# Kernel optimization log

Hardware: AMD Instinct MI355X
Metric: run time of the kernel (lower is better)

The kernel has to match this reference:

```python
import jax, jax.numpy as jnp
import numpy as np

BIT_W = 8   # config.bit_wt
BIT_A = 8   # config.bit_act (activations sliced 2 bits at a time)
STRIDE = (1, 1)
PAD = 1


def _conv(a, w):
    # NCHW input, OIHW weight, stride 1, symmetric padding 1 (matches wrapped Conv2d)
    return jax.lax.conv_general_dilated(
        a, w, window_strides=STRIDE, padding=[(PAD, PAD), (PAD, PAD)],
        dimension_numbers=("NCHW", "OIHW", "NCHW"))


def setup_inputs() -> dict:
    key = jax.random.key(0)
    k1, k2, k3 = jax.random.split(key, 3)
    x = jax.random.normal(k1, (64, 64, 56, 56), dtype=jnp.float32)
    weight = jax.random.normal(k2, (64, 64, 3, 3), dtype=jnp.float32)
    bias = jax.random.normal(k3, (64,), dtype=jnp.float32)
    scale_a = jnp.full((1,), 20.0, dtype=jnp.float32)      # conv_q.scale
    scale_w = jnp.full((1,), 20.0, dtype=jnp.float32)      # wrapped_module.weight_scale
    zero_point = jnp.full((1,), -128.0, dtype=jnp.float32)  # conv_q.zero_point
    return {"x": x, "weight": weight, "bias": bias,
            "scale_a": scale_a, "scale_w": scale_w, "zero_point": zero_point}


def reference(x, weight, bias, scale_a, scale_w, zero_point):
    sa = scale_a[0]
    sw = scale_w[0]
    zp = zero_point[0]
    # activation quantization: round(x*scale_a - zero_point), clamp to [0, 2^bit_act - 1]
    q_in = jnp.clip(jnp.round(x * sa - zp), 0.0, 2.0 ** BIT_A - 1.0)
    # weight quantization: round(w * scale_w), interpreted in two's complement
    q_w = jnp.round(weight * sw)
    w_off = q_w + 2.0 ** BIT_W  # (w + (1 << bit_weight)) before bit masking

    acc = jnp.zeros((), dtype=jnp.float32)
    for ba in range(BIT_A // 2):
        # 2-bit activation slice: (a >> 2*ba) & 3
        a_sl = jnp.mod(jnp.floor(q_in / (4.0 ** ba)), 4.0)
        for bw in range(BIT_W):
            # weight bit bw: ((w + 2^B) >> bw) & 1
            w_bit = jnp.mod(jnp.floor(w_off / (2.0 ** bw)), 2.0)
            r = _conv(a_sl, w_bit)
            sgn = -1.0 if bw == BIT_W - 1 else 1.0  # MSB = sign bit (two's complement)
            acc = acc + sgn * (2.0 ** (2 * ba + bw)) * r

    # zero-point correction: conv(ones * zp, q_w) added back (no-op when zp == 0)
    acc = acc + zp * _conv(jnp.ones_like(q_in), q_w)

    out = acc / (sw * sa) + bias[None, :, None, None]
    return out
```

## Files before the change

kernel.cpp:

```cpp
#include <hip/hip_runtime.h>


typedef int v4i __attribute__((ext_vector_type(4)));

#define QA_ROW   3712
#define QA_IMG   215296
#define QA_BYTES 13778944

__global__ __launch_bounds__(64) void prep_wq(const float* __restrict__ wt,
                                              const float* __restrict__ sw_p,
                                              signed char* __restrict__ w8,
                                              int* __restrict__ Qtc,
                                              int* __restrict__ Qraw) {
  const int o = blockIdx.x;
  const int i = threadIdx.x;
  const float sw = sw_p[0];
  const float* wp = wt + (size_t)(o * 64 + i) * 9;
  int q[9];
#pragma unroll
  for (int k = 0; k < 9; ++k) q[k] = (int)rintf(wp[k] * sw);
#pragma unroll
  for (int k = 0; k < 9; ++k)
    w8[(o * 9 + k) * 64 + i] = (signed char)(q[k] & 255);
#pragma unroll
  for (int k = 0; k < 9; ++k) {
    int stc = (int)(signed char)(q[k] & 255);
    int srw = q[k];
#pragma unroll
    for (int off = 32; off; off >>= 1) {
      stc += __shfl_xor(stc, off);
      srw += __shfl_xor(srw, off);
    }
    if (i == 0) { Qtc[o * 9 + k] = stc; Qraw[o * 9 + k] = srw; }
  }
}

__global__ __launch_bounds__(256) void quant_a(const float* __restrict__ x,
                                               const float* __restrict__ sa_p,
                                               const float* __restrict__ zp_p,
                                               signed char* __restrict__ qa) {
  __shared__ int ldsbuf[1904];
  signed char* lds = (signed char*)ldsbuf;
  const int bx = blockIdx.x;
  const int n = blockIdx.y;
  const int t = threadIdx.x;
  const float sa = sa_p[0], zp = zp_p[0];
  const float* xim = x + (size_t)n * 200704;
  const int h0 = bx * 2;

#pragma unroll
  for (int it = 0; it < 7; ++it) {
    const int idx = t + 256 * it;
    const int r = idx >= 896;
    const int rem = idx - 896 * r;
    const int c = (rem * 2341) >> 15;
    const int w4 = rem - c * 14;
    const float4 v = *(const float4*)(xim + (size_t)c * 3136 + (h0 + r) * 56 + w4 * 4);
    signed char* dst = lds + r * 3808 + w4 * 272 + c;
    const float vv[4] = {v.x, v.y, v.z, v.w};
#pragma unroll
    for (int e = 0; e < 4; ++e) {
      float tq;
      {
#pragma clang fp contract(off)
        tq = vv[e] * sa - zp;
      }
      float qf = rintf(tq);
      qf = fminf(fmaxf(qf, 0.0f), 255.0f);
      dst[e * 68] = (signed char)((int)qf - 128);
    }
  }
  __syncthreads();

  signed char* const qim = qa + (size_t)n * QA_IMG;
#pragma unroll
  for (int it = 0; it < 2; ++it) {
    const int idx = t + 256 * it;
    if (idx < 448) {
      const int r = idx >= 224;
      const int u = idx - 224 * r;
      const int w = u >> 2, q2 = u & 3;
      const unsigned* s = (const unsigned*)(lds + r * 3808 + w * 68 + q2 * 16);
      const uint4 vv = make_uint4(s[0], s[1], s[2], s[3]);
      *((uint4*)(qim + (size_t)(h0 + r + 1) * QA_ROW + (w + 1) * 64 + q2 * 16)) = vv;
    } else if (idx < 464) {
      const int p = idx - 448;
      const int r = p >> 3;
      const int side = (p >> 2) & 1;
      const int j = p & 3;
      *((uint4*)(qim + (size_t)(h0 + r + 1) * QA_ROW + side * 57 * 64 + j * 16)) =
          make_uint4(0, 0, 0, 0);
    }
  }
  if (bx == 0 && t < 232)
    ((uint4*)qim)[t] = make_uint4(0, 0, 0, 0);
  if (bx == 27 && t < 232)
    ((uint4*)(qim + (size_t)57 * QA_ROW))[t] = make_uint4(0, 0, 0, 0);
}

__global__ __launch_bounds__(256, 4) void conv_mfma(
    const signed char* __restrict__ qa, const signed char* __restrict__ w8,
    const int* __restrict__ Qtc, const int* __restrict__ Qraw,
    const float* __restrict__ bias, const float* __restrict__ sa_p,
    const float* __restrict__ sw_p, const float* __restrict__ zp_p,
    float* __restrict__ out) {
  const int tid = threadIdx.x;
  const int lane = tid & 63;
  const int og = tid >> 6;
  const int n = blockIdx.y;
  const int p0 = blockIdx.x * 64;
  const int ln = lane & 15;
  const int kg = lane >> 4;
  const int o = og * 16 + ln;

  const signed char* wbp = w8 + (size_t)o * 576 + kg * 16;
  v4i B[9];
#pragma unroll
  for (int tp = 0; tp < 9; ++tp) B[tp] = *(const v4i*)(wbp + tp * 64);

  const float sa = sa_p[0], sw = sw_p[0], zp = zp_p[0];
  float ct[9];
#pragma unroll
  for (int k = 0; k < 9; ++k)
    ct[k] = 128.0f * (float)Qtc[o * 9 + k] + zp * (float)Qraw[o * 9 + k];
  const float Full = ct[0] + ct[1] + ct[2] + ct[3] + ct[4] + ct[5] + ct[6] + ct[7] + ct[8];
  const float Rtop = ct[0] + ct[1] + ct[2];
  const float Rbot = ct[6] + ct[7] + ct[8];
  const float Clft = ct[0] + ct[3] + ct[6];
  const float Crgt = ct[2] + ct[5] + ct[8];
  const float c0 = ct[0], c2 = ct[2], c6 = ct[6], c8 = ct[8];
  const float rden = 1.0f / (sw * sa);
  const float bo = bias[o];

  const signed char* qim = qa + (size_t)n * QA_IMG + kg * 16;
  float* const obase = out + (size_t)(n * 64 + o) * 3136;

#pragma unroll 1
  for (int t = 0; t < 4; ++t) {
    const int pxa = p0 + t * 16 + ln;
    const int hp = (pxa * 9363) >> 19;
    const int wp = pxa - hp * 56;
    const signed char* abase = qim + (hp * 58 + wp) * 64;
    v4i A[9];
#pragma unroll
    for (int kh = 0; kh < 3; ++kh)
#pragma unroll
      for (int kw = 0; kw < 3; ++kw)
        A[kh * 3 + kw] = *(const v4i*)(abase + kh * QA_ROW + kw * 64);

    v4i acc = {0, 0, 0, 0};
#pragma unroll
    for (int k = 0; k < 9; ++k)
      acc = __builtin_amdgcn_mfma_i32_16x16x64_i8(A[k], B[k], acc, 0, 0, 0);

    const int pxb = p0 + t * 16 + kg * 4;
    const int hb = (pxb * 9363) >> 19;
    const int wb2 = pxb - hb * 56;
    float tmp[4];
    if (hb >= 1 && hb <= 54 && wb2 >= 1 && wb2 <= 51) {
#pragma unroll
      for (int e = 0; e < 4; ++e)
        tmp[e] = ((float)acc[e] + Full) * rden + bo;
    } else {
#pragma unroll
      for (int e = 0; e < 4; ++e) {
        const int p = pxb + e;
        const int h = (p * 9363) >> 19;
        const int w = p - h * 56;
        const bool tb = (h == 0), bb = (h == 55), lb = (w == 0), rb = (w == 55);
        float corr = Full;
        corr -= tb ? Rtop : 0.0f;
        corr -= bb ? Rbot : 0.0f;
        corr -= lb ? Clft : 0.0f;
        corr -= rb ? Crgt : 0.0f;
        corr += (tb && lb) ? c0 : 0.0f;
        corr += (tb && rb) ? c2 : 0.0f;
        corr += (bb && lb) ? c6 : 0.0f;
        corr += (bb && rb) ? c8 : 0.0f;
        tmp[e] = ((float)acc[e] + corr) * rden + bo;
      }
    }
    float4 vv;
    vv.x = tmp[0]; vv.y = tmp[1]; vv.z = tmp[2]; vv.w = tmp[3];
    *(float4*)(obase + pxb) = vv;
  }
}

extern "C" void kernel_launch(void* const* d_in, const int* in_sizes, int n_in,
                              void* d_out, int out_size, void* d_ws, size_t ws_size,
                              hipStream_t stream) {
  const float* x    = (const float*)d_in[0];
  const float* wt   = (const float*)d_in[1];
  const float* bias = (const float*)d_in[2];
  const float* sa   = (const float*)d_in[3];
  const float* sw   = (const float*)d_in[4];
  const float* zp   = (const float*)d_in[5];
  float* out = (float*)d_out;

  char* ws = (char*)d_ws;
  signed char* qa = (signed char*)ws;
  signed char* w8 = (signed char*)(ws + QA_BYTES);
  int* Qtc  = (int*)(ws + QA_BYTES + 36864);
  int* Qraw = (int*)(ws + QA_BYTES + 36864 + 2304);

  prep_wq<<<64, 64, 0, stream>>>(wt, sw, w8, Qtc, Qraw);
  quant_a<<<dim3(28, 64), 256, 0, stream>>>(x, sa, zp, qa);
  conv_mfma<<<dim3(49, 64), 256, 0, stream>>>(qa, w8, Qtc, Qraw, bias, sa, sw, zp, out);
}
```

Baseline: 145.8 us.

## Stage activation row tile in LDS and compute two output-channel groups per wave

The conv kernel now copies a 6-row padded int8 activation tile, plus a precomputed 9-case border correction table, into LDS. Each wave reuses every activation fragment across two 16-channel weight sets, and the block covers 4 output rows. This removes the redundant global loads of the 3x3 overlapping window and the per-block border-correction arithmetic, at the cost of 24 KB of LDS per block, twice as many resident B registers, and fewer blocks (14x64). The prep kernel now builds the zero-point/border correction table directly.

```diff
diff --git a/kernel.cpp b/kernel.cpp
--- a/kernel.cpp
+++ b/kernel.cpp
@@ -9,9 +9,9 @@
 
 __global__ __launch_bounds__(64) void prep_wq(const float* __restrict__ wt,
                                               const float* __restrict__ sw_p,
+                                              const float* __restrict__ zp_p,
                                               signed char* __restrict__ w8,
-                                              int* __restrict__ Qtc,
-                                              int* __restrict__ Qraw) {
+                                              float* __restrict__ corr_tab) {
   const int o = blockIdx.x;
   const int i = threadIdx.x;
   const float sw = sw_p[0];
@@ -22,16 +22,31 @@
 #pragma unroll
   for (int k = 0; k < 9; ++k)
     w8[(o * 9 + k) * 64 + i] = (signed char)(q[k] & 255);
+
+  int stc[9], srw[9];
 #pragma unroll
   for (int k = 0; k < 9; ++k) {
-    int stc = (int)(signed char)(q[k] & 255);
-    int srw = q[k];
+    int a = (int)(signed char)(q[k] & 255);
+    int b = q[k];
 #pragma unroll
     for (int off = 32; off; off >>= 1) {
-      stc += __shfl_xor(stc, off);
-      srw += __shfl_xor(srw, off);
-    }
-    if (i == 0) { Qtc[o * 9 + k] = stc; Qraw[o * 9 + k] = srw; }
+      a += __shfl_xor(a, off);
+      b += __shfl_xor(b, off);
+    }
+    stc[k] = a; srw[k] = b;
+  }
+  const float zp = zp_p[0];
+  if (i < 9) {
+    const int v = i / 3, hc = i % 3;
+    float corr = 0.0f;
+#pragma unroll
+    for (int k = 0; k < 9; ++k) {
+      const int kh = k / 3, kw = k % 3;
+      const bool drop = (v == 1 && kh == 0) || (v == 2 && kh == 2) ||
+                        (hc == 1 && kw == 0) || (hc == 2 && kw == 2);
+      if (!drop) corr += 128.0f * (float)stc[k] + zp * (float)srw[k];
+    }
+    corr_tab[i * 64 + o] = corr;
   }
 }
 
@@ -100,89 +115,92 @@
 
 __global__ __launch_bounds__(256, 4) void conv_mfma(
     const signed char* __restrict__ qa, const signed char* __restrict__ w8,
-    const int* __restrict__ Qtc, const int* __restrict__ Qraw,
-    const float* __restrict__ bias, const float* __restrict__ sa_p,
-    const float* __restrict__ sw_p, const float* __restrict__ zp_p,
+    const float* __restrict__ corr_tab, const float* __restrict__ bias,
+    const float* __restrict__ sa_p, const float* __restrict__ sw_p,
     float* __restrict__ out) {
+  __shared__ __align__(16) signed char lds[24576];
   const int tid = threadIdx.x;
+  const int n = blockIdx.y;
+  const int h0 = blockIdx.x * 4;
+
+  {
+    const uint4* src = (const uint4*)(qa + (size_t)n * QA_IMG + (size_t)h0 * QA_ROW);
+    const uint4* csrc = (const uint4*)corr_tab;
+    uint4* dst = (uint4*)lds;
+#pragma unroll
+    for (int it = 0; it < 6; ++it) {
+      const int idx = tid + it * 256;
+      uint4 v;
+      if (idx < 1392) v = src[idx];
+      else v = csrc[idx - 1392];
+      dst[idx] = v;
+    }
+  }
+  __syncthreads();
+
   const int lane = tid & 63;
-  const int og = tid >> 6;
-  const int n = blockIdx.y;
-  const int p0 = blockIdx.x * 64;
+  const int wv = tid >> 6;
+  const int phalf = wv & 1;
+  const int ogp = wv >> 1;
   const int ln = lane & 15;
   const int kg = lane >> 4;
-  const int o = og * 16 + ln;
-
-  const signed char* wbp = w8 + (size_t)o * 576 + kg * 16;
-  v4i B[9];
-#pragma unroll
-  for (int tp = 0; tp < 9; ++tp) B[tp] = *(const v4i*)(wbp + tp * 64);
-
-  const float sa = sa_p[0], sw = sw_p[0], zp = zp_p[0];
-  float ct[9];
-#pragma unroll
-  for (int k = 0; k < 9; ++k)
-    ct[k] = 128.0f * (float)Qtc[o * 9 + k] + zp * (float)Qraw[o * 9 + k];
-  const float Full = ct[0] + ct[1] + ct[2] + ct[3] + ct[4] + ct[5] + ct[6] + ct[7] + ct[8];
-  const float Rtop = ct[0] + ct[1] + ct[2];
-  const float Rbot = ct[6] + ct[7] + ct[8];
-  const float Clft = ct[0] + ct[3] + ct[6];
-  const float Crgt = ct[2] + ct[5] + ct[8];
-  const float c0 = ct[0], c2 = ct[2], c6 = ct[6], c8 = ct[8];
+  const int oa = ogp * 32 + ln;
+
+  const signed char* wba = w8 + (size_t)oa * 576 + kg * 16;
+  v4i Ba[9], Bb[9];
+#pragma unroll
+  for (int t = 0; t < 9; ++t) {
+    Ba[t] = *(const v4i*)(wba + t * 64);
+    Bb[t] = *(const v4i*)(wba + 9216 + t * 64);
+  }
+
+  const float sa = sa_p[0], sw = sw_p[0];
   const float rden = 1.0f / (sw * sa);
-  const float bo = bias[o];
-
-  const signed char* qim = qa + (size_t)n * QA_IMG + kg * 16;
-  float* const obase = out + (size_t)(n * 64 + o) * 3136;
+  const float boa = bias[oa], bob = bias[oa + 16];
+  const float* ctab = (const float*)(lds + 22272);
+  const float cFa = ctab[oa];
+  const float cFb = ctab[oa + 16];
+  float* const outa = out + (size_t)(n * 64 + oa) * 3136 + h0 * 56;
+  float* const outb = outa + 16 * 3136;
 
 #pragma unroll 1
-  for (int t = 0; t < 4; ++t) {
-    const int pxa = p0 + t * 16 + ln;
-    const int hp = (pxa * 9363) >> 19;
-    const int wp = pxa - hp * 56;
-    const signed char* abase = qim + (hp * 58 + wp) * 64;
-    v4i A[9];
-#pragma unroll
-    for (int kh = 0; kh < 3; ++kh)
-#pragma unroll
-      for (int kw = 0; kw < 3; ++kw)
-        A[kh * 3 + kw] = *(const v4i*)(abase + kh * QA_ROW + kw * 64);
-
-    v4i acc = {0, 0, 0, 0};
-#pragma unroll
-    for (int k = 0; k < 9; ++k)
-      acc = __builtin_amdgcn_mfma_i32_16x16x64_i8(A[k], B[k], acc, 0, 0, 0);
-
-    const int pxb = p0 + t * 16 + kg * 4;
-    const int hb = (pxb * 9363) >> 19;
-    const int wb2 = pxb - hb * 56;
-    float tmp[4];
-    if (hb >= 1 && hb <= 54 && wb2 >= 1 && wb2 <= 51) {
-#pragma unroll
-      for (int e = 0; e < 4; ++e)
-        tmp[e] = ((float)acc[e] + Full) * rden + bo;
-    } else {
-#pragma unroll
-      for (int e = 0; e < 4; ++e) {
-        const int p = pxb + e;
-        const int h = (p * 9363) >> 19;
-        const int w = p - h * 56;
-        const bool tb = (h == 0), bb = (h == 55), lb = (w == 0), rb = (w == 55);
-        float corr = Full;
-        corr -= tb ? Rtop : 0.0f;
-        corr -= bb ? Rbot : 0.0f;
-        corr -= lb ? Clft : 0.0f;
-        corr -= rb ? Crgt : 0.0f;
-        corr += (tb && lb) ? c0 : 0.0f;
-        corr += (tb && rb) ? c2 : 0.0f;
-        corr += (bb && lb) ? c6 : 0.0f;
-        corr += (bb && rb) ? c8 : 0.0f;
-        tmp[e] = ((float)acc[e] + corr) * rden + bo;
+  for (int t = 0; t < 7; ++t) {
+    const int pb = phalf * 112 + t * 16;
+    const int pa = pb + ln;
+    const int hr = (pa * 9363) >> 19;
+    const int wc = pa - hr * 56;
+    const signed char* ab = lds + (hr * 58 + wc) * 64 + kg * 16;
+    v4i acca = {0, 0, 0, 0}, accb = {0, 0, 0, 0};
+#pragma unroll
+    for (int kh = 0; kh < 3; ++kh) {
+#pragma unroll
+      for (int kw = 0; kw < 3; ++kw) {
+        const v4i A = *(const v4i*)(ab + (kh * 58 + kw) * 64);
+        acca = __builtin_amdgcn_mfma_i32_16x16x64_i8(A, Ba[kh * 3 + kw], acca, 0, 0, 0);
+        accb = __builtin_amdgcn_mfma_i32_16x16x64_i8(A, Bb[kh * 3 + kw], accb, 0, 0, 0);
       }
     }
-    float4 vv;
-    vv.x = tmp[0]; vv.y = tmp[1]; vv.z = tmp[2]; vv.w = tmp[3];
-    *(float4*)(obase + pxb) = vv;
+    const int pxb = pb + kg * 4;
+    float ta[4], tb[4];
+#pragma unroll
+    for (int e = 0; e < 4; ++e) {
+      const int p = pxb + e;
+      const int hh = (p * 9363) >> 19;
+      const int ww = p - hh * 56;
+      const int hg = h0 + hh;
+      float ca = cFa, cb = cFb;
+      if ((hg == 0) | (hg == 55) | (ww == 0) | (ww == 55)) {
+        const int vcase = (hg == 0) ? 1 : ((hg == 55) ? 2 : 0);
+        const int hcase = (ww == 0) ? 1 : ((ww == 55) ? 2 : 0);
+        const int cidx = (vcase * 3 + hcase) * 64;
+        ca = ctab[cidx + oa];
+        cb = ctab[cidx + oa + 16];
+      }
+      ta[e] = ((float)acca[e] + ca) * rden + boa;
+      tb[e] = ((float)accb[e] + cb) * rden + bob;
+    }
+    *(float4*)(outa + pxb) = make_float4(ta[0], ta[1], ta[2], ta[3]);
+    *(float4*)(outb + pxb) = make_float4(tb[0], tb[1], tb[2], tb[3]);
   }
 }
 
@@ -200,10 +218,9 @@
   char* ws = (char*)d_ws;
   signed char* qa = (signed char*)ws;
   signed char* w8 = (signed char*)(ws + QA_BYTES);
-  int* Qtc  = (int*)(ws + QA_BYTES + 36864);
-  int* Qraw = (int*)(ws + QA_BYTES + 36864 + 2304);
-
-  prep_wq<<<64, 64, 0, stream>>>(wt, sw, w8, Qtc, Qraw);
+  float* corr_tab = (float*)(ws + QA_BYTES + 36864);
+
+  prep_wq<<<64, 64, 0, stream>>>(wt, sw, zp, w8, corr_tab);
   quant_a<<<dim3(28, 64), 256, 0, stream>>>(x, sa, zp, qa);
-  conv_mfma<<<dim3(49, 64), 256, 0, stream>>>(qa, w8, Qtc, Qraw, bias, sa, sw, zp, out);
-}
+  conv_mfma<<<dim3(14, 64), 256, 0, stream>>>(qa, w8, corr_tab, bias, sa, sw, out);
+}
```

After: 124.9 us. 14.4% less time.
